# Optimization experiments

Hardware: AMD Instinct MI355X
Metric: run time of the kernel (lower is better)

The kernel has to match this reference:

```python
import jax, jax.numpy as jnp
import numpy as np

DIM = 768
HEADS = 12
HEAD_DIM = DIM // HEADS
B, N = 8, 1024


def setup_inputs() -> dict:
    key = jax.random.key(0)
    ks = jax.random.split(key, 5)
    x = jax.random.normal(ks[0], (B, N, DIM), dtype=jnp.float32)
    shared_rel_pos = jax.random.normal(ks[1], (HEADS, N, N), dtype=jnp.float32)
    qkv_w = jax.random.normal(ks[2], (3 * DIM, DIM), dtype=jnp.float32) * (DIM ** -0.5)
    proj_w = jax.random.normal(ks[3], (DIM, DIM), dtype=jnp.float32) * (DIM ** -0.5)
    proj_b = jnp.zeros((DIM,), dtype=jnp.float32)
    return {"x": x, "shared_rel_pos": shared_rel_pos, "qkv_w": qkv_w,
            "proj_w": proj_w, "proj_b": proj_b}


def reference(x, shared_rel_pos, qkv_w, proj_w, proj_b):
    Bt, Nt, C = x.shape
    scale = HEAD_DIM ** -0.5
    # qkv: Linear(dim, 3*dim, bias=False) -> (B, N, 3, H, hd) -> (3, B, H, N, hd)
    qkv = jnp.einsum('bnc,oc->bno', x, qkv_w)
    qkv = qkv.reshape(Bt, Nt, 3, HEADS, HEAD_DIM).transpose(2, 0, 3, 1, 4)
    q, k, v = qkv[0], qkv[1], qkv[2]
    # scaled dot-product attention with shared relative-position bias
    attn = jnp.einsum('bhqd,bhkd->bhqk', q, k) * scale
    attn = attn + shared_rel_pos[None]  # broadcast over batch
    attn = jax.nn.softmax(attn, axis=-1)
    out = jnp.einsum('bhqk,bhkd->bhqd', attn, v)
    out = out.transpose(0, 2, 1, 3).reshape(Bt, Nt, C)
    return jnp.einsum('bnc,oc->bno', out, proj_w) + proj_b
```

## Files before the change

kernel.cpp:

```cpp
#include <hip/hip_runtime.h>
#include <hip/hip_bf16.h>
#include <stdint.h>

#define HEADS 12
#define HD 64
#define SEQ 1024
#define CDIM 768
#define LOG2E 1.44269504f

typedef __attribute__((ext_vector_type(8))) short bfrag;
typedef __attribute__((ext_vector_type(4))) float facc;
typedef __attribute__((ext_vector_type(4))) _Float16 h4;
typedef __attribute__((ext_vector_type(2))) __fp16 pk2;

__device__ __forceinline__ ushort f2bf(float f) {
    union { float f; uint32_t u; } v; v.f = f;
    uint32_t u = v.u;
    uint32_t r = (u + 0x7FFFu + ((u >> 16) & 1u)) >> 16;
    return (ushort)r;
}
__device__ __forceinline__ ushort f2h(float f) {
    union { _Float16 h; ushort u; } c; c.h = (_Float16)f; return c.u;
}
__device__ __forceinline__ h4 pack4h(float p0, float p1, float p2, float p3) {
    union { h4 v4; pk2 v2[2]; } u;
    u.v2[0] = __builtin_amdgcn_cvt_pkrtz(p0, p1);
    u.v2[1] = __builtin_amdgcn_cvt_pkrtz(p2, p3);
    return u.v4;
}

__global__ void cvt_all(const float* __restrict__ x, const float* __restrict__ qw,
                        const float* __restrict__ pw,
                        ushort* __restrict__ xd, ushort* __restrict__ qd,
                        ushort* __restrict__ pd) {
    long i = ((long)blockIdx.x * 256 + threadIdx.x) * 4;
    if (i < 6291456) {
        float4 v = *(const float4*)(x + i);
        ushort4 o = {f2bf(v.x), f2bf(v.y), f2bf(v.z), f2bf(v.w)};
        *(ushort4*)(xd + i) = o;
    } else if (i < 8060928) {
        long j = i - 6291456;
        float4 v = *(const float4*)(qw + j);
        ushort4 o = {f2bf(v.x), f2bf(v.y), f2bf(v.z), f2bf(v.w)};
        *(ushort4*)(qd + j) = o;
    } else if (i < 8650752) {
        long j = i - 8060928;
        float4 v = *(const float4*)(pw + j);
        ushort4 o = {f2bf(v.x), f2bf(v.y), f2bf(v.z), f2bf(v.w)};
        *(ushort4*)(pd + j) = o;
    }
}

#define GLOAD16(gsrc, ldst) \
    __builtin_amdgcn_global_load_lds((const __attribute__((address_space(1))) uint32_t*)(gsrc), \
                                     (__attribute__((address_space(3))) uint32_t*)(ldst), 16, 0, 0)

template<int EPI>
__global__ __launch_bounds__(256) void gemm_nt(
    const ushort* __restrict__ A, const ushort* __restrict__ Bm,
    ushort* __restrict__ qb, ushort* __restrict__ kb, ushort* __restrict__ vb,
    const float* __restrict__ projb, float* __restrict__ out)
{
    __shared__ ushort As[128 * 32];
    __shared__ ushort Bs[128 * 32];
    const int t = threadIdx.x;
    const int w = t >> 6, l = t & 63;
    const int wm = w >> 1, wn = w & 1;
    const int lr = l & 15, lg = l >> 4;
    const int m0 = blockIdx.x * 128;
    const int o0 = blockIdx.y * 128;

    facc acc[4][4] = {};

    const int srow = w * 16 + (l >> 2);
    const int scol = (l & 3) * 8;
    const ushort* Ag = A + (size_t)(m0 + srow) * CDIM + scol;
    const ushort* Bg = Bm + (size_t)(o0 + srow) * CDIM + scol;

    for (int k0 = 0; k0 < CDIM; k0 += 32) {
        __syncthreads();
        GLOAD16(Ag + k0,             As + w * 512);
        GLOAD16(Ag + 64 * CDIM + k0, As + 2048 + w * 512);
        GLOAD16(Bg + k0,             Bs + w * 512);
        GLOAD16(Bg + 64 * CDIM + k0, Bs + 2048 + w * 512);
        __syncthreads();
        bfrag af[4], bf[4];
#pragma unroll
        for (int m = 0; m < 4; ++m)
            af[m] = *(const bfrag*)&As[(wm * 64 + m * 16 + lr) * 32 + lg * 8];
#pragma unroll
        for (int n = 0; n < 4; ++n)
            bf[n] = *(const bfrag*)&Bs[(wn * 64 + n * 16 + lr) * 32 + lg * 8];
#pragma unroll
        for (int m = 0; m < 4; ++m)
#pragma unroll
            for (int n = 0; n < 4; ++n)
                acc[m][n] = __builtin_amdgcn_mfma_f32_16x16x32_bf16(af[m], bf[n], acc[m][n], 0, 0, 0);
    }

    if (EPI == 0) {
        const int tsel = o0 / CDIM;
        const int h_base = (o0 % CDIM) / 64;
        ushort* dst = (tsel == 0) ? qb : ((tsel == 1) ? kb : vb);
        const float scl = (tsel == 0) ? 0.18033688f : 1.0f;
#pragma unroll
        for (int m = 0; m < 4; ++m) {
            int grow = m0 + wm * 64 + m * 16 + lg * 4;
#pragma unroll
            for (int n = 0; n < 4; ++n) {
                int h = h_base + wn;
                int d = n * 16 + lr;
#pragma unroll
                for (int r = 0; r < 4; ++r) {
                    int row = grow + r;
                    int b = row >> 10, nn = row & 1023;
                    ushort val = (tsel == 2) ? f2h(acc[m][n][r])
                                             : f2bf(acc[m][n][r] * scl);
                    dst[(((size_t)(b * HEADS + h)) * SEQ + nn) * HD + d] = val;
                }
            }
        }
    } else {
#pragma unroll
        for (int m = 0; m < 4; ++m) {
            int grow = m0 + wm * 64 + m * 16 + lg * 4;
#pragma unroll
            for (int n = 0; n < 4; ++n) {
                int o = o0 + wn * 64 + n * 16 + lr;
                float bias = projb[o];
#pragma unroll
                for (int r = 0; r < 4; ++r)
                    out[(size_t)(grow + r) * CDIM + o] = acc[m][n][r] + bias;
            }
        }
    }
}

__global__ __launch_bounds__(256, 3) void attn_kernel(
    const ushort* __restrict__ qbuf, const ushort* __restrict__ kbuf,
    const ushort* __restrict__ vbuf, const float* __restrict__ biasf,
    ushort* __restrict__ attn_out)
{
    __shared__ ushort Ks[2][64 * 72];
    __shared__ ushort Vt[2][64 * 72];

    const int t = threadIdx.x;
    const int w = t >> 6, l = t & 63;
    const int lr = l & 15, lg = l >> 4;

    const int bid = blockIdx.x;
    const int lid = (bid & 7) * 96 + (bid >> 3);
    const int h  = lid >> 6;
    const int qt = (lid >> 3) & 7;
    const int b  = lid & 7;

    const int q0 = qt * 128;
    const size_t headoff = (size_t)(b * HEADS + h) * SEQ * HD;
    const int qrb = q0 + w * 32;

    bfrag aQ[2][2];
#pragma unroll
    for (int n = 0; n < 2; ++n) {
        const ushort* Qp = qbuf + headoff + (size_t)(qrb + n * 16 + lr) * HD;
        aQ[n][0] = *(const bfrag*)(Qp + lg * 8);
        aQ[n][1] = *(const bfrag*)(Qp + 32 + lg * 8);
    }

    float mrun[2] = {-1e30f, -1e30f}, lrun[2] = {0.0f, 0.0f};
    facc Ov[2][4] = {};

    const float* bprow[2];
#pragma unroll
    for (int n = 0; n < 2; ++n)
        bprow[n] = biasf + ((size_t)h * SEQ + qrb + n * 16 + lr) * SEQ;

    const int krow = t >> 3, kc = (t & 7) * 8;
    const int p2 = t & 31, vg_ = t >> 5;
    const ushort* kgb = kbuf + headoff + (size_t)krow * HD + kc;
    const ushort* vgb = vbuf + headoff + (size_t)(2 * p2) * HD + vg_ * 8;

    bfrag krA = *(const bfrag*)(kgb);
    bfrag krB = *(const bfrag*)(kgb + (size_t)32 * HD);
    bfrag vrA = *(const bfrag*)(vgb);
    bfrag vrB = *(const bfrag*)(vgb + HD);
    float4 bcur[2][4];
#pragma unroll
    for (int n = 0; n < 2; ++n)
#pragma unroll
        for (int c = 0; c < 4; ++c)
            bcur[n][c] = *(const float4*)(bprow[n] + c * 16 + lg * 4);

    *(bfrag*)&Ks[0][krow * 72 + kc] = krA;
    *(bfrag*)&Ks[0][(krow + 32) * 72 + kc] = krB;
#pragma unroll
    for (int i = 0; i < 8; ++i) {
        uint32_t pk = (uint32_t)(uint16_t)vrA[i] | ((uint32_t)(uint16_t)vrB[i] << 16);
        *(uint32_t*)&Vt[0][(vg_ * 8 + i) * 72 + 2 * p2] = pk;
    }
    krA = *(const bfrag*)(kgb + (size_t)64 * HD);
    krB = *(const bfrag*)(kgb + (size_t)96 * HD);
    vrA = *(const bfrag*)(vgb + (size_t)64 * HD);
    vrB = *(const bfrag*)(vgb + (size_t)65 * HD);
    __syncthreads();

    for (int tt = 0; tt < 16; ++tt) {
        const int cur = tt & 1;
        const ushort* Kc = Ks[cur];
        const ushort* Vc = Vt[cur];

        facc St[2][4];
        h4 pf[2][4];
        float psum[2] = {0.0f, 0.0f};
        float pmax[2] = {-3.0e38f, -3.0e38f};
#pragma unroll
        for (int c = 0; c < 4; ++c) {
            bfrag kf0 = *(const bfrag*)&Kc[(c * 16 + lr) * 72 + lg * 8];
            bfrag kf1 = *(const bfrag*)&Kc[(c * 16 + lr) * 72 + 32 + lg * 8];
#pragma unroll
            for (int n = 0; n < 2; ++n) {
                float4 bb = bcur[n][c];
                facc s;
                s[0] = bb.x * LOG2E; s[1] = bb.y * LOG2E;
                s[2] = bb.z * LOG2E; s[3] = bb.w * LOG2E;
                __builtin_amdgcn_s_setprio(1);
                s = __builtin_amdgcn_mfma_f32_16x16x32_bf16(kf0, aQ[n][0], s, 0, 0, 0);
                s = __builtin_amdgcn_mfma_f32_16x16x32_bf16(kf1, aQ[n][1], s, 0, 0, 0);
                __builtin_amdgcn_s_setprio(0);
                St[n][c] = s;
                float p0 = exp2f(s[0] - mrun[n]);
                float p1 = exp2f(s[1] - mrun[n]);
                float p2f = exp2f(s[2] - mrun[n]);
                float p3 = exp2f(s[3] - mrun[n]);
                psum[n] += (p0 + p1) + (p2f + p3);
                pmax[n] = fmaxf(pmax[n], fmaxf(fmaxf(s[0], s[1]), fmaxf(s[2], s[3])));
                pf[n][c] = pack4h(p0, p1, p2f, p3);
            }
        }

        if (tt < 15) {
            const int kvn = (tt + 1) << 6;
#pragma unroll
            for (int n = 0; n < 2; ++n)
#pragma unroll
                for (int c = 0; c < 4; ++c)
                    bcur[n][c] = *(const float4*)(bprow[n] + kvn + c * 16 + lg * 4);
        }

#pragma unroll
        for (int n = 0; n < 2; ++n) {
            pmax[n] = fmaxf(pmax[n], __shfl_xor(pmax[n], 16));
            pmax[n] = fmaxf(pmax[n], __shfl_xor(pmax[n], 32));
        }
        int ok = (pmax[0] <= mrun[0] + 11.541560f) && (pmax[1] <= mrun[1] + 11.541560f);
        if (!__all(ok)) {
#pragma unroll
            for (int n = 0; n < 2; ++n) {
                float mnew = fmaxf(mrun[n], pmax[n]);
                float al = exp2f(mrun[n] - mnew);
                psum[n] = 0.0f;
#pragma unroll
                for (int c = 0; c < 4; ++c) {
                    float p0 = exp2f(St[n][c][0] - mnew);
                    float p1 = exp2f(St[n][c][1] - mnew);
                    float p2f = exp2f(St[n][c][2] - mnew);
                    float p3 = exp2f(St[n][c][3] - mnew);
                    psum[n] += (p0 + p1) + (p2f + p3);
                    pf[n][c] = pack4h(p0, p1, p2f, p3);
                }
#pragma unroll
                for (int r = 0; r < 4; ++r) {
                    float a = __shfl(al, lg * 4 + r);
#pragma unroll
                    for (int d = 0; d < 4; ++d) Ov[n][d][r] *= a;
                }
                lrun[n] *= al;
                mrun[n] = mnew;
            }
        }
#pragma unroll
        for (int n = 0; n < 2; ++n) {
            psum[n] += __shfl_xor(psum[n], 16);
            psum[n] += __shfl_xor(psum[n], 32);
            lrun[n] += psum[n];
        }

        if (tt < 15) {
            *(bfrag*)&Ks[cur ^ 1][krow * 72 + kc] = krA;
            *(bfrag*)&Ks[cur ^ 1][(krow + 32) * 72 + kc] = krB;
#pragma unroll
            for (int i = 0; i < 8; ++i) {
                uint32_t pk = (uint32_t)(uint16_t)vrA[i] | ((uint32_t)(uint16_t)vrB[i] << 16);
                *(uint32_t*)&Vt[cur ^ 1][(vg_ * 8 + i) * 72 + 2 * p2] = pk;
            }
        }
        if (tt < 14) {
            const int kvn = (tt + 2) << 6;
            krA = *(const bfrag*)(kgb + (size_t)kvn * HD);
            krB = *(const bfrag*)(kgb + (size_t)(kvn + 32) * HD);
            vrA = *(const bfrag*)(vgb + (size_t)kvn * HD);
            vrB = *(const bfrag*)(vgb + (size_t)(kvn + 1) * HD);
        }

        __builtin_amdgcn_s_setprio(1);
#pragma unroll
        for (int d0 = 0; d0 < 4; ++d0) {
#pragma unroll
            for (int c = 0; c < 4; ++c) {
                h4 bv = *(const h4*)&Vc[(d0 * 16 + lr) * 72 + c * 16 + lg * 4];
#pragma unroll
                for (int n = 0; n < 2; ++n)
                    Ov[n][d0] = __builtin_amdgcn_mfma_f32_16x16x16f16(pf[n][c], bv, Ov[n][d0], 0, 0, 0);
            }
        }
        __builtin_amdgcn_s_setprio(0);

        if (tt < 15) __syncthreads();
    }

#pragma unroll
    for (int n = 0; n < 2; ++n) {
        ushort* op = attn_out + ((size_t)b * SEQ + qrb + n * 16) * CDIM + h * HD;
#pragma unroll
        for (int r = 0; r < 4; ++r) {
            float ll = __shfl(lrun[n], lg * 4 + r);
            float rl = 1.0f / ll;
#pragma unroll
            for (int d = 0; d < 4; ++d)
                op[(size_t)(lg * 4 + r) * CDIM + d * 16 + lr] = f2bf(Ov[n][d][r] * rl);
        }
    }
}

extern "C" void kernel_launch(void* const* d_in, const int* in_sizes, int n_in,
                              void* d_out, int out_size, void* d_ws, size_t ws_size,
                              hipStream_t stream) {
    const float* x     = (const float*)d_in[0];
    const float* rel   = (const float*)d_in[1];
    const float* qkvw  = (const float*)d_in[2];
    const float* projw = (const float*)d_in[3];
    const float* projb = (const float*)d_in[4];
    float* out = (float*)d_out;

    char* ws = (char*)d_ws;
    ushort* qb    = (ushort*)(ws);
    ushort* kb    = (ushort*)(ws + 12582912);
    ushort* vb    = (ushort*)(ws + 25165824);
    ushort* attnb = (ushort*)(ws + 37748736);
    ushort* xbf   = attnb;
    ushort* wbf   = (ushort*)(ws + 50331648);
    ushort* pwbf  = (ushort*)(ws + 53870592);

    cvt_all<<<8448, 256, 0, stream>>>(x, qkvw, projw, xbf, wbf, pwbf);

    gemm_nt<0><<<dim3(64, 18), 256, 0, stream>>>(xbf, wbf, qb, kb, vb, nullptr, nullptr);
    attn_kernel<<<768, 256, 0, stream>>>(qb, kb, vb, rel, attnb);
    gemm_nt<1><<<dim3(64, 6), 256, 0, stream>>>(attnb, pwbf, nullptr, nullptr, nullptr, projb, out);
}
```

Measured before the change: 148.8 us.

## Precompute fp16 log2e-scaled bias in QKV GEMM and skip max shuffles

Adds extra blocks to the QKV GEMM launch that convert the fp32 relative-position bias into fp16 pre-multiplied by log2e. The attention kernel then reads half-width bias, which halves the bias bytes it streams for every batch. The online-softmax rescale check now uses per-lane maxima with a looser threshold, so cross-lane reductions happen only when a rescale is needed. The trade-off is an extra conversion pass over the bias, a larger workspace, and reduced bias precision with a wider fp16 dynamic range for probabilities.

```diff
diff --git a/kernel.cpp b/kernel.cpp
--- a/kernel.cpp
+++ b/kernel.cpp
@@ -21,6 +21,9 @@
 }
 __device__ __forceinline__ ushort f2h(float f) {
     union { _Float16 h; ushort u; } c; c.h = (_Float16)f; return c.u;
+}
+__device__ __forceinline__ float h2f(uint32_t u16) {
+    union { _Float16 h; ushort u; } c; c.u = (ushort)u16; return (float)c.h;
 }
 __device__ __forceinline__ h4 pack4h(float p0, float p1, float p2, float p3) {
     union { h4 v4; pk2 v2[2]; } u;
@@ -59,11 +62,25 @@
 __global__ __launch_bounds__(256) void gemm_nt(
     const ushort* __restrict__ A, const ushort* __restrict__ Bm,
     ushort* __restrict__ qb, ushort* __restrict__ kb, ushort* __restrict__ vb,
-    const float* __restrict__ projb, float* __restrict__ out)
+    const float* __restrict__ projb, float* __restrict__ out,
+    const float* __restrict__ relf, ushort* __restrict__ biash)
 {
     __shared__ ushort As[128 * 32];
     __shared__ ushort Bs[128 * 32];
     const int t = threadIdx.x;
+
+    if (EPI == 0 && blockIdx.y >= 18) {
+        long cb = (long)(blockIdx.y - 18) * 64 + blockIdx.x;
+        long i = (cb * 256 + t) * 4;
+        if (i < 12582912) {
+            float4 v = *(const float4*)(relf + i);
+            ushort4 o = {f2h(v.x * LOG2E), f2h(v.y * LOG2E),
+                         f2h(v.z * LOG2E), f2h(v.w * LOG2E)};
+            *(ushort4*)(biash + i) = o;
+        }
+        return;
+    }
+
     const int w = t >> 6, l = t & 63;
     const int wm = w >> 1, wn = w & 1;
     const int lr = l & 15, lg = l >> 4;
@@ -138,7 +155,7 @@
 
 __global__ __launch_bounds__(256, 3) void attn_kernel(
     const ushort* __restrict__ qbuf, const ushort* __restrict__ kbuf,
-    const ushort* __restrict__ vbuf, const float* __restrict__ biasf,
+    const ushort* __restrict__ vbuf, const ushort* __restrict__ biash,
     ushort* __restrict__ attn_out)
 {
     __shared__ ushort Ks[2][64 * 72];
@@ -169,10 +186,10 @@
     float mrun[2] = {-1e30f, -1e30f}, lrun[2] = {0.0f, 0.0f};
     facc Ov[2][4] = {};
 
-    const float* bprow[2];
+    const ushort* bprow[2];
 #pragma unroll
     for (int n = 0; n < 2; ++n)
-        bprow[n] = biasf + ((size_t)h * SEQ + qrb + n * 16 + lr) * SEQ;
+        bprow[n] = biash + ((size_t)h * SEQ + qrb + n * 16 + lr) * SEQ;
 
     const int krow = t >> 3, kc = (t & 7) * 8;
     const int p2 = t & 31, vg_ = t >> 5;
@@ -183,12 +200,12 @@
     bfrag krB = *(const bfrag*)(kgb + (size_t)32 * HD);
     bfrag vrA = *(const bfrag*)(vgb);
     bfrag vrB = *(const bfrag*)(vgb + HD);
-    float4 bcur[2][4];
+    uint2 bcur[2][4];
 #pragma unroll
     for (int n = 0; n < 2; ++n)
 #pragma unroll
         for (int c = 0; c < 4; ++c)
-            bcur[n][c] = *(const float4*)(bprow[n] + c * 16 + lg * 4);
+            bcur[n][c] = *(const uint2*)(bprow[n] + c * 16 + lg * 4);
 
     *(bfrag*)&Ks[0][krow * 72 + kc] = krA;
     *(bfrag*)&Ks[0][(krow + 32) * 72 + kc] = krB;
@@ -218,10 +235,12 @@
             bfrag kf1 = *(const bfrag*)&Kc[(c * 16 + lr) * 72 + 32 + lg * 8];
 #pragma unroll
             for (int n = 0; n < 2; ++n) {
-                float4 bb = bcur[n][c];
+                uint2 bb = bcur[n][c];
                 facc s;
-                s[0] = bb.x * LOG2E; s[1] = bb.y * LOG2E;
-                s[2] = bb.z * LOG2E; s[3] = bb.w * LOG2E;
+                s[0] = h2f(bb.x & 0xffffu);
+                s[1] = h2f(bb.x >> 16);
+                s[2] = h2f(bb.y & 0xffffu);
+                s[3] = h2f(bb.y >> 16);
                 __builtin_amdgcn_s_setprio(1);
                 s = __builtin_amdgcn_mfma_f32_16x16x32_bf16(kf0, aQ[n][0], s, 0, 0, 0);
                 s = __builtin_amdgcn_mfma_f32_16x16x32_bf16(kf1, aQ[n][1], s, 0, 0, 0);
@@ -243,19 +262,17 @@
             for (int n = 0; n < 2; ++n)
 #pragma unroll
                 for (int c = 0; c < 4; ++c)
-                    bcur[n][c] = *(const float4*)(bprow[n] + kvn + c * 16 + lg * 4);
-        }
-
-#pragma unroll
-        for (int n = 0; n < 2; ++n) {
-            pmax[n] = fmaxf(pmax[n], __shfl_xor(pmax[n], 16));
-            pmax[n] = fmaxf(pmax[n], __shfl_xor(pmax[n], 32));
-        }
-        int ok = (pmax[0] <= mrun[0] + 11.541560f) && (pmax[1] <= mrun[1] + 11.541560f);
-        if (!__all(ok)) {
+                    bcur[n][c] = *(const uint2*)(bprow[n] + kvn + c * 16 + lg * 4);
+        }
+
+        int viol = (pmax[0] > mrun[0] + 14.0f) || (pmax[1] > mrun[1] + 14.0f);
+        if (__any(viol)) {
 #pragma unroll
             for (int n = 0; n < 2; ++n) {
-                float mnew = fmaxf(mrun[n], pmax[n]);
+                float pm = pmax[n];
+                pm = fmaxf(pm, __shfl_xor(pm, 16));
+                pm = fmaxf(pm, __shfl_xor(pm, 32));
+                float mnew = fmaxf(mrun[n], pm);
                 float al = exp2f(mrun[n] - mnew);
                 psum[n] = 0.0f;
 #pragma unroll
@@ -342,17 +359,18 @@
     float* out = (float*)d_out;
 
     char* ws = (char*)d_ws;
-    ushort* qb    = (ushort*)(ws);
-    ushort* kb    = (ushort*)(ws + 12582912);
-    ushort* vb    = (ushort*)(ws + 25165824);
-    ushort* attnb = (ushort*)(ws + 37748736);
+    ushort* biash = (ushort*)(ws);
+    ushort* qb    = (ushort*)(ws + 25165824);
+    ushort* kb    = (ushort*)(ws + 37748736);
+    ushort* vb    = (ushort*)(ws + 50331648);
+    ushort* attnb = (ushort*)(ws + 62914560);
     ushort* xbf   = attnb;
-    ushort* wbf   = (ushort*)(ws + 50331648);
-    ushort* pwbf  = (ushort*)(ws + 53870592);
+    ushort* wbf   = (ushort*)(ws + 75497472);
+    ushort* pwbf  = (ushort*)(ws + 79036416);
 
     cvt_all<<<8448, 256, 0, stream>>>(x, qkvw, projw, xbf, wbf, pwbf);
 
-    gemm_nt<0><<<dim3(64, 18), 256, 0, stream>>>(xbf, wbf, qb, kb, vb, nullptr, nullptr);
-    attn_kernel<<<768, 256, 0, stream>>>(qb, kb, vb, rel, attnb);
-    gemm_nt<1><<<dim3(64, 6), 256, 0, stream>>>(attnb, pwbf, nullptr, nullptr, nullptr, projb, out);
-}
+    gemm_nt<0><<<dim3(64, 210), 256, 0, stream>>>(xbf, wbf, qb, kb, vb, nullptr, nullptr, rel, biash);
+    attn_kernel<<<768, 256, 0, stream>>>(qb, kb, vb, biash, attnb);
+    gemm_nt<1><<<dim3(64, 6), 256, 0, stream>>>(attnb, pwbf, nullptr, nullptr, nullptr, projb, out, nullptr, nullptr);
+}
```

Result: no change. 150.6 us (+1.2%).
